# Optimization experiments

Measured on AMD Instinct MI355X. Metric: run time of the kernel, lower is better.

The kernel has to match this reference:

```python
import jax, jax.numpy as jnp
import numpy as np

N = 50000      # nodes
E = 800000     # edges
F_IN = 256
H1, D1 = 4, 32   # conv1 heads, per-head dim (hidden_features)
H2, D2 = 1, 32   # conv2 heads, per-head dim (out_features)
NEG_SLOPE = 0.2


def setup_inputs():
    key = jax.random.key(0)
    ks = jax.random.split(key, 12)
    x = jax.random.normal(ks[0], (N, F_IN), dtype=jnp.float32)
    src = jax.random.randint(ks[1], (E,), 0, N, dtype=jnp.int32)
    dst = jax.random.randint(ks[2], (E,), 0, N, dtype=jnp.int32)
    s = 0.05
    W1 = jax.random.normal(ks[3], (F_IN, H1 * D1), dtype=jnp.float32) * s
    al1 = jax.random.normal(ks[4], (H1, D1), dtype=jnp.float32) * s
    ar1 = jax.random.normal(ks[5], (H1, D1), dtype=jnp.float32) * s
    b1 = jnp.zeros((H1 * D1,), dtype=jnp.float32)
    W2 = jax.random.normal(ks[6], (H1 * D1, H2 * D2), dtype=jnp.float32) * s
    al2 = jax.random.normal(ks[7], (H2, D2), dtype=jnp.float32) * s
    ar2 = jax.random.normal(ks[8], (H2, D2), dtype=jnp.float32) * s
    b2 = jnp.zeros((H2 * D2,), dtype=jnp.float32)
    return {"x": x, "W1": W1, "al1": al1, "ar1": ar1, "b1": b1,
            "W2": W2, "al2": al2, "ar2": ar2, "b2": b2,
            "src": src, "dst": dst}


def gat_layer(x, W, al, ar, b, src, dst, H, D):
    # x: [N, F] -> feat: [N, H, D]
    feat = (x @ W).reshape(-1, H, D)
    el = jnp.sum(feat * al, axis=-1)   # [N, H]
    er = jnp.sum(feat * ar, axis=-1)   # [N, H]
    # per-edge attention logits, LeakyReLU
    e = jax.nn.leaky_relu(el[src] + er[dst], negative_slope=NEG_SLOPE)  # [E, H]
    # edge softmax over destination neighborhoods (stable)
    m = jax.ops.segment_max(e, dst, num_segments=N)          # [N, H]
    m = jnp.where(jnp.isfinite(m), m, 0.0)                   # guard zero-in-degree
    ee = jnp.exp(e - m[dst])                                 # [E, H]
    z = jax.ops.segment_sum(ee, dst, num_segments=N)         # [N, H]
    a = ee / jnp.maximum(z[dst], 1e-16)                      # [E, H]
    # weighted message aggregation
    msg = feat[src] * a[:, :, None]                          # [E, H, D]
    rst = jax.ops.segment_sum(msg, dst, num_segments=N)      # [N, H, D]
    return (rst + b.reshape(1, H, D)).reshape(-1, H * D)     # flatten(1)


def reference(x, W1, al1, ar1, b1, W2, al2, ar2, b2, src, dst):
    # dropouts are identity in eval mode; is_out_layer=True => no activation
    h = gat_layer(x, W1, al1, ar1, b1, src, dst, H1, D1)     # [N, H1*D1]
    out = gat_layer(h, W2, al2, ar2, b2, src, dst, H2, D2)   # [N, H2*D2]
    return out
```

## Files before the change

### kernel.cpp

```cpp
#include <hip/hip_runtime.h>

constexpr int F_IN = 256;
constexpr int H1 = 4, D1 = 32, F1 = H1 * D1;
constexpr int H2 = 1, D2 = 32, F2 = H2 * D2;
constexpr float NEG = 0.2f;

constexpr int BW = 128;
constexpr int NBUK_MAX = 512;
constexpr int CB = 128;

typedef short short8 __attribute__((ext_vector_type(8)));
typedef float f32x4 __attribute__((ext_vector_type(4)));

__device__ inline float bf2f(unsigned short u) {
    unsigned int x = ((unsigned int)u) << 16;
    return __builtin_bit_cast(float, x);
}
__device__ inline unsigned short f2bf(float f) {
    __bf16 h = (__bf16)f;
    return __builtin_bit_cast(unsigned short, h);
}

__global__ __launch_bounds__(256) void chist(const int* __restrict__ dst,
                                             unsigned int* __restrict__ Hc,
                                             int E, int nbuk) {
    __shared__ unsigned int h[NBUK_MAX];
    int tid = threadIdx.x;
    for (int i = tid; i < nbuk; i += 256) h[i] = 0;
    __syncthreads();
    int epb = (E + CB - 1) / CB;
    int e0 = blockIdx.x * epb, e1 = min(e0 + epb, E);
    for (int e = e0 + tid; e < e1; e += 256)
        atomicAdd(&h[dst[e] / BW], 1u);
    __syncthreads();
    for (int i = tid; i < nbuk; i += 256) Hc[(size_t)blockIdx.x * nbuk + i] = h[i];
}

__global__ __launch_bounds__(512) void bscan(const unsigned int* __restrict__ Hc,
                                             unsigned int* __restrict__ Bb,
                                             unsigned int* __restrict__ S, int nbuk) {
    __shared__ unsigned int tot[NBUK_MAX];
    int t = threadIdx.x;
    unsigned int run = 0;
    if (t < nbuk) {
        for (int b = 0; b < CB; ++b) {
            Bb[(size_t)b * nbuk + t] = run;
            run += Hc[(size_t)b * nbuk + t];
        }
    }
    tot[t] = (t < nbuk) ? run : 0;
    __syncthreads();
    for (int o = 1; o < NBUK_MAX; o <<= 1) {
        unsigned int v = (t >= o) ? tot[t - o] : 0;
        __syncthreads();
        tot[t] += v;
        __syncthreads();
    }
    if (t < nbuk) S[t] = tot[t] - run;
    if (t == nbuk - 1) S[nbuk] = tot[t];
}

__global__ __launch_bounds__(256) void cscat(const int* __restrict__ src,
                                             const int* __restrict__ dst,
                                             const unsigned int* __restrict__ Bb,
                                             const unsigned int* __restrict__ S,
                                             int2* __restrict__ pairs, int E, int nbuk) {
    __shared__ unsigned int h[NBUK_MAX];
    int tid = threadIdx.x;
    for (int i = tid; i < nbuk; i += 256) h[i] = 0;
    __syncthreads();
    int epb = (E + CB - 1) / CB;
    int e0 = blockIdx.x * epb, e1 = min(e0 + epb, E);
    const unsigned int* bb = Bb + (size_t)blockIdx.x * nbuk;
    for (int e = e0 + tid; e < e1; e += 256) {
        int d = dst[e];
        int k = d / BW;
        unsigned int r = atomicAdd(&h[k], 1u);
        unsigned int p = S[k] + bb[k] + r;
        pairs[p] = make_int2(src[e], d);
    }
}

__global__ __launch_bounds__(256) void fscat(const int2* __restrict__ pairs,
                                             const unsigned int* __restrict__ S,
                                             int* __restrict__ off, int* __restrict__ csr,
                                             int n, int E) {
    int k = blockIdx.x;
    int tid = threadIdx.x;
    unsigned int s0 = S[k], s1 = S[k + 1];
    __shared__ unsigned int cnt[BW];
    __shared__ unsigned int ex[BW];
    if (tid < BW) cnt[tid] = 0;
    __syncthreads();
    for (unsigned int i = s0 + tid; i < s1; i += 256)
        atomicAdd(&cnt[pairs[i].y - k * BW], 1u);
    __syncthreads();
    unsigned int orig = (tid < BW) ? cnt[tid] : 0;
    if (tid < BW) ex[tid] = orig;
    __syncthreads();
    for (int o = 1; o < BW; o <<= 1) {
        unsigned int v = (tid < BW && tid >= (unsigned)o) ? ex[tid - o] : 0;
        __syncthreads();
        if (tid < BW) ex[tid] += v;
        __syncthreads();
    }
    if (tid < BW) {
        ex[tid] -= orig;
        int node = k * BW + tid;
        if (node < n) off[node] = (int)(s0 + ex[tid]);
    }
    if (tid < BW) cnt[tid] = 0;
    __syncthreads();
    for (unsigned int i = s0 + tid; i < s1; i += 256) {
        int2 pr = pairs[i];
        int loc = pr.y - k * BW;
        unsigned int r = atomicAdd(&cnt[loc], 1u);
        csr[s0 + ex[loc] + r] = pr.x;
    }
    if (k == 0 && tid == 0) off[n] = E;
}

__global__ void wsplit_swz(const float* __restrict__ W,
                           unsigned short* __restrict__ Wh,
                           unsigned short* __restrict__ Wl, int K, int C) {
    int idx = blockIdx.x * 256 + threadIdx.x;
    if (idx >= K * C) return;
    int j    = idx & 7;
    int lane = (idx >> 3) & 63;
    int t    = idx >> 9;
    int FC   = C >> 4;
    int fc   = t % FC, ks = t / FC;
    int k = ks * 32 + (lane >> 4) * 8 + j;
    int c = fc * 16 + (lane & 15);
    float v = W[(size_t)k * C + c];
    __bf16 h = (__bf16)v;
    float hv = (float)h;
    __bf16 lo = (__bf16)(v - hv);
    Wh[idx] = __builtin_bit_cast(unsigned short, h);
    Wl[idx] = __builtin_bit_cast(unsigned short, lo);
}

constexpr int BM1 = 32;
__global__ __launch_bounds__(256) void gemm1_mfma(
    const float* __restrict__ X,
    const unsigned short* __restrict__ Wh,
    const unsigned short* __restrict__ Wl,
    unsigned short* __restrict__ outb, int n)
{
    __shared__ float xs[64 * BM1 * 4];
    const int tid  = threadIdx.x;
    const int lane = tid & 63;
    const int wid  = tid >> 6;
    const int wrow = (wid >> 1) * 16;
    const int wcol = (wid & 1) * 64;
    const int wc16 = wcol >> 4;
    const int row0 = blockIdx.x * BM1;
    const int l16  = lane & 15;
    const int khi  = lane >> 4;

    {
        int r = lane & 31;
        int sub = lane >> 5;
        int gr = row0 + r;
        gr = gr < n ? gr : (n - 1);
        const float* rowp = X + (size_t)gr * F_IN;
#pragma unroll
        for (int i = 0; i < 8; ++i) {
            int kc = wid * 16 + i * 2;
            const float* src = rowp + (kc + sub) * 4;
            float* dstf = &xs[kc * BM1 * 4];
            __builtin_amdgcn_global_load_lds(
                (const __attribute__((address_space(1))) unsigned int*)src,
                (__attribute__((address_space(3))) unsigned int*)dstf,
                16, 0, 0);
        }
    }
    asm volatile("s_waitcnt vmcnt(0)" ::: "memory");
    __syncthreads();

    f32x4 acc[4];
#pragma unroll
    for (int ni = 0; ni < 4; ++ni) acc[ni] = f32x4{0.f, 0.f, 0.f, 0.f};

    const int rt = wrow + l16;

#pragma unroll
    for (int ks = 0; ks < 8; ++ks) {
        const int kc = ks * 8 + khi * 2;

        short8 bh[4], bl[4];
#pragma unroll
        for (int ni = 0; ni < 4; ++ni) {
            int base = ((ks * 8 + wc16 + ni) * 64 + lane) * 8;
            bh[ni] = *(const short8*)(Wh + base);
            bl[ni] = *(const short8*)(Wl + base);
        }

        float4 xa0 = *(const float4*)&xs[(kc + 0) * BM1 * 4 + rt * 4];
        float4 xa1 = *(const float4*)&xs[(kc + 1) * BM1 * 4 + rt * 4];
        float v[8] = {xa0.x, xa0.y, xa0.z, xa0.w, xa1.x, xa1.y, xa1.z, xa1.w};
        short8 ah, al;
#pragma unroll
        for (int j = 0; j < 8; ++j) {
            __bf16 h = (__bf16)v[j];
            float hv = (float)h;
            __bf16 lo = (__bf16)(v[j] - hv);
            ah[j] = __builtin_bit_cast(short, h);
            al[j] = __builtin_bit_cast(short, lo);
        }

#pragma unroll
        for (int ni = 0; ni < 4; ++ni) {
            acc[ni] = __builtin_amdgcn_mfma_f32_16x16x32_bf16(al, bh[ni], acc[ni], 0, 0, 0);
            acc[ni] = __builtin_amdgcn_mfma_f32_16x16x32_bf16(ah, bl[ni], acc[ni], 0, 0, 0);
            acc[ni] = __builtin_amdgcn_mfma_f32_16x16x32_bf16(ah, bh[ni], acc[ni], 0, 0, 0);
        }
    }

    int rbase = row0 + wrow + khi * 4;
#pragma unroll
    for (int rr = 0; rr < 4; ++rr) {
        int row = rbase + rr;
        if (row < n) {
#pragma unroll
            for (int ni = 0; ni < 4; ++ni)
                outb[(size_t)row * F1 + wcol + ni * 16 + l16] = f2bf(acc[ni][rr]);
        }
    }
}

constexpr int BM2 = 64;
__global__ __launch_bounds__(256) void gemm2_mfma(
    const float* __restrict__ X,
    const unsigned short* __restrict__ Wh,
    const unsigned short* __restrict__ Wl,
    float* __restrict__ out, int n)
{
    __shared__ float xs[32 * BM2 * 4];
    const int tid  = threadIdx.x;
    const int lane = tid & 63;
    const int wid  = tid >> 6;
    const int wrow = wid * 16;
    const int row0 = blockIdx.x * BM2;
    const int l16  = lane & 15;
    const int khi  = lane >> 4;

    {
        int gr = row0 + lane;
        gr = gr < n ? gr : (n - 1);
        const float* rowp = X + (size_t)gr * F1;
#pragma unroll
        for (int i = 0; i < 8; ++i) {
            int kc = wid * 8 + i;
            const float* src = rowp + kc * 4;
            float* dstf = &xs[kc * BM2 * 4];
            __builtin_amdgcn_global_load_lds(
                (const __attribute__((address_space(1))) unsigned int*)src,
                (__attribute__((address_space(3))) unsigned int*)dstf,
                16, 0, 0);
        }
    }
    asm volatile("s_waitcnt vmcnt(0)" ::: "memory");
    __syncthreads();

    f32x4 acc[2];
#pragma unroll
    for (int ni = 0; ni < 2; ++ni) acc[ni] = f32x4{0.f, 0.f, 0.f, 0.f};

    const int rt = wrow + l16;

#pragma unroll
    for (int ks = 0; ks < 4; ++ks) {
        const int kc = ks * 8 + khi * 2;

        short8 bh[2], bl[2];
#pragma unroll
        for (int ni = 0; ni < 2; ++ni) {
            int base = ((ks * 2 + ni) * 64 + lane) * 8;
            bh[ni] = *(const short8*)(Wh + base);
            bl[ni] = *(const short8*)(Wl + base);
        }

        float4 xa0 = *(const float4*)&xs[(kc + 0) * BM2 * 4 + rt * 4];
        float4 xa1 = *(const float4*)&xs[(kc + 1) * BM2 * 4 + rt * 4];
        float v[8] = {xa0.x, xa0.y, xa0.z, xa0.w, xa1.x, xa1.y, xa1.z, xa1.w};
        short8 ah, al;
#pragma unroll
        for (int j = 0; j < 8; ++j) {
            __bf16 h = (__bf16)v[j];
            float hv = (float)h;
            __bf16 lo = (__bf16)(v[j] - hv);
            ah[j] = __builtin_bit_cast(short, h);
            al[j] = __builtin_bit_cast(short, lo);
        }

#pragma unroll
        for (int ni = 0; ni < 2; ++ni) {
            acc[ni] = __builtin_amdgcn_mfma_f32_16x16x32_bf16(al, bh[ni], acc[ni], 0, 0, 0);
            acc[ni] = __builtin_amdgcn_mfma_f32_16x16x32_bf16(ah, bl[ni], acc[ni], 0, 0, 0);
            acc[ni] = __builtin_amdgcn_mfma_f32_16x16x32_bf16(ah, bh[ni], acc[ni], 0, 0, 0);
        }
    }

    int rbase = row0 + wrow + khi * 4;
#pragma unroll
    for (int rr = 0; rr < 4; ++rr) {
        int row = rbase + rr;
        if (row < n) {
#pragma unroll
            for (int ni = 0; ni < 2; ++ni)
                out[(size_t)row * F2 + ni * 16 + l16] = acc[ni][rr];
        }
    }
}

template <int F, int H>
__global__ __launch_bounds__(256) void elr_bf16(const unsigned short* __restrict__ featb,
                                                const float* __restrict__ al,
                                                const float* __restrict__ ar,
                                                float* __restrict__ el,
                                                float* __restrict__ er, int n)
{
    constexpr int LPN = F / 4;
    constexpr int NPW = 64 / LPN;
    int wid = (blockIdx.x * 256 + threadIdx.x) >> 6;
    int lane = threadIdx.x & 63;
    int node = wid * NPW + lane / LPN;
    int l2 = lane % LPN;
    int c0 = l2 * 4;
    if (node >= n) return;
    ushort4 u = *(const ushort4*)(featb + (size_t)node * F + c0);
    float f0 = bf2f(u.x), f1 = bf2f(u.y), f2 = bf2f(u.z), f3 = bf2f(u.w);
    float4 a = *(const float4*)(al + c0);
    float4 r = *(const float4*)(ar + c0);
    float pel = f0 * a.x + f1 * a.y + f2 * a.z + f3 * a.w;
    float per = f0 * r.x + f1 * r.y + f2 * r.z + f3 * r.w;
#pragma unroll
    for (int o = 1; o < 8; o <<= 1) {
        pel += __shfl_xor(pel, o);
        per += __shfl_xor(per, o);
    }
    if ((l2 & 7) == 0) {
        int h = c0 / 32;
        el[(size_t)node * H + h] = pel;
        er[(size_t)node * H + h] = per;
    }
}

template <int F, int H>
__global__ __launch_bounds__(256) void elr_kernel(const float* __restrict__ feat,
                                                  const float* __restrict__ al,
                                                  const float* __restrict__ ar,
                                                  float* __restrict__ el,
                                                  float* __restrict__ er, int n)
{
    constexpr int LPN = F / 2;
    constexpr int NPW = 64 / LPN;
    int wid = (blockIdx.x * 256 + threadIdx.x) >> 6;
    int lane = threadIdx.x & 63;
    int node = wid * NPW + lane / LPN;
    int l2 = lane % LPN;
    int c0 = l2 * 2;
    if (node >= n) return;
    float2 f = *(const float2*)(feat + (size_t)node * F + c0);
    float2 a = *(const float2*)(al + c0);
    float2 r = *(const float2*)(ar + c0);
    float pel = f.x * a.x + f.y * a.y;
    float per = f.x * r.x + f.y * r.y;
#pragma unroll
    for (int o = 1; o < 16; o <<= 1) {
        pel += __shfl_xor(pel, o);
        per += __shfl_xor(per, o);
    }
    if ((l2 & 15) == 0) {
        int h = c0 / 32;
        el[(size_t)node * H + h] = pel;
        er[(size_t)node * H + h] = per;
    }
}

__global__ __launch_bounds__(256) void agg1_kernel(
    const int* __restrict__ off, const int* __restrict__ csr_src,
    const unsigned short* __restrict__ featb, const float* __restrict__ el,
    const float* __restrict__ er, const float* __restrict__ b,
    float* __restrict__ out, int n)
{
    int wid = (blockIdx.x * 256 + threadIdx.x) >> 6;
    int lane = threadIdx.x & 63;
    if (wid >= n) return;
    int c0 = (lane & 31) * 4;
    int h = (lane & 31) >> 3;
    int half = lane >> 5;
    float erv = er[(size_t)wid * H1 + h];
    float sw = 0.f;
    float4 acc = {0.f, 0.f, 0.f, 0.f};
    int jb = off[wid], je = off[wid + 1];
    int j = jb + half;
    for (; j + 6 < je; j += 8) {
        int s0 = csr_src[j];
        int s1 = csr_src[j + 2];
        int s2 = csr_src[j + 4];
        int s3 = csr_src[j + 6];
        ushort4 u0 = *(const ushort4*)(featb + (size_t)s0 * F1 + c0);
        ushort4 u1 = *(const ushort4*)(featb + (size_t)s1 * F1 + c0);
        ushort4 u2 = *(const ushort4*)(featb + (size_t)s2 * F1 + c0);
        ushort4 u3 = *(const ushort4*)(featb + (size_t)s3 * F1 + c0);
        float t0 = el[(size_t)s0 * H1 + h] + erv;
        float t1 = el[(size_t)s1 * H1 + h] + erv;
        float t2 = el[(size_t)s2 * H1 + h] + erv;
        float t3 = el[(size_t)s3 * H1 + h] + erv;
        t0 = t0 > 0.f ? t0 : NEG * t0;
        t1 = t1 > 0.f ? t1 : NEG * t1;
        t2 = t2 > 0.f ? t2 : NEG * t2;
        t3 = t3 > 0.f ? t3 : NEG * t3;
        float w0 = __expf(t0), w1 = __expf(t1), w2 = __expf(t2), w3 = __expf(t3);
        sw += (w0 + w1) + (w2 + w3);
        acc.x = fmaf(w0, bf2f(u0.x), fmaf(w1, bf2f(u1.x), fmaf(w2, bf2f(u2.x), fmaf(w3, bf2f(u3.x), acc.x))));
        acc.y = fmaf(w0, bf2f(u0.y), fmaf(w1, bf2f(u1.y), fmaf(w2, bf2f(u2.y), fmaf(w3, bf2f(u3.y), acc.y))));
        acc.z = fmaf(w0, bf2f(u0.z), fmaf(w1, bf2f(u1.z), fmaf(w2, bf2f(u2.z), fmaf(w3, bf2f(u3.z), acc.z))));
        acc.w = fmaf(w0, bf2f(u0.w), fmaf(w1, bf2f(u1.w), fmaf(w2, bf2f(u2.w), fmaf(w3, bf2f(u3.w), acc.w))));
    }
    for (; j < je; j += 2) {
        int s = csr_src[j];
        ushort4 u = *(const ushort4*)(featb + (size_t)s * F1 + c0);
        float t = el[(size_t)s * H1 + h] + erv;
        t = t > 0.f ? t : NEG * t;
        float w = __expf(t);
        sw += w;
        acc.x = fmaf(w, bf2f(u.x), acc.x);
        acc.y = fmaf(w, bf2f(u.y), acc.y);
        acc.z = fmaf(w, bf2f(u.z), acc.z);
        acc.w = fmaf(w, bf2f(u.w), acc.w);
    }
    acc.x += __shfl_xor(acc.x, 32);
    acc.y += __shfl_xor(acc.y, 32);
    acc.z += __shfl_xor(acc.z, 32);
    acc.w += __shfl_xor(acc.w, 32);
    sw    += __shfl_xor(sw, 32);
    if (half == 0) {
        float inv = 1.f / fmaxf(sw, 1e-16f);
        float4 bb = *(const float4*)(b + c0);
        float4 t = {acc.x * inv + bb.x, acc.y * inv + bb.y,
                    acc.z * inv + bb.z, acc.w * inv + bb.w};
        *(float4*)(out + (size_t)wid * F1 + c0) = t;
    }
}

__global__ __launch_bounds__(256) void agg2_kernel(
    const int* __restrict__ off, const int* __restrict__ csr_src,
    const float* __restrict__ feat, const float* __restrict__ el,
    const float* __restrict__ er, const float* __restrict__ b,
    float* __restrict__ out, int n)
{
    int wid = (blockIdx.x * 256 + threadIdx.x) >> 6;
    int lane = threadIdx.x & 63;
    if (wid >= n) return;
    int c0 = (lane & 7) * 4;
    int grp = lane >> 3;
    float erv = er[wid];
    float sw = 0.f;
    float4 acc = {0.f, 0.f, 0.f, 0.f};
    int jb = off[wid], je = off[wid + 1];
    int j = jb + grp;
    for (; j + 8 < je; j += 16) {
        int s0 = csr_src[j];
        int s1 = csr_src[j + 8];
        float4 f0 = *(const float4*)(feat + (size_t)s0 * F2 + c0);
        float4 f1 = *(const float4*)(feat + (size_t)s1 * F2 + c0);
        float t0 = el[s0] + erv;
        float t1 = el[s1] + erv;
        t0 = t0 > 0.f ? t0 : NEG * t0;
        t1 = t1 > 0.f ? t1 : NEG * t1;
        float w0 = __expf(t0);
        float w1 = __expf(t1);
        sw += w0 + w1;
        acc.x = fmaf(w0, f0.x, fmaf(w1, f1.x, acc.x));
        acc.y = fmaf(w0, f0.y, fmaf(w1, f1.y, acc.y));
        acc.z = fmaf(w0, f0.z, fmaf(w1, f1.z, acc.z));
        acc.w = fmaf(w0, f0.w, fmaf(w1, f1.w, acc.w));
    }
    for (; j < je; j += 8) {
        int s = csr_src[j];
        float4 f = *(const float4*)(feat + (size_t)s * F2 + c0);
        float t = el[s] + erv;
        t = t > 0.f ? t : NEG * t;
        float w = __expf(t);
        sw += w;
        acc.x = fmaf(w, f.x, acc.x);
        acc.y = fmaf(w, f.y, acc.y);
        acc.z = fmaf(w, f.z, acc.z);
        acc.w = fmaf(w, f.w, acc.w);
    }
#pragma unroll
    for (int o = 8; o < 64; o <<= 1) {
        acc.x += __shfl_xor(acc.x, o);
        acc.y += __shfl_xor(acc.y, o);
        acc.z += __shfl_xor(acc.z, o);
        acc.w += __shfl_xor(acc.w, o);
        sw    += __shfl_xor(sw, o);
    }
    if (lane < 8) {
        float inv = 1.f / fmaxf(sw, 1e-16f);
        float4 bb = *(const float4*)(b + c0);
        float4 t = {acc.x * inv + bb.x, acc.y * inv + bb.y,
                    acc.z * inv + bb.z, acc.w * inv + bb.w};
        *(float4*)(out + (size_t)wid * F2 + c0) = t;
    }
}

extern "C" void kernel_launch(void* const* d_in, const int* in_sizes, int n_in,
                              void* d_out, int out_size, void* d_ws, size_t ws_size,
                              hipStream_t stream) {
    const float* x   = (const float*)d_in[0];
    const float* W1  = (const float*)d_in[1];
    const float* al1 = (const float*)d_in[2];
    const float* ar1 = (const float*)d_in[3];
    const float* b1  = (const float*)d_in[4];
    const float* W2  = (const float*)d_in[5];
    const float* al2 = (const float*)d_in[6];
    const float* ar2 = (const float*)d_in[7];
    const float* b2  = (const float*)d_in[8];
    const int*   src = (const int*)d_in[9];
    const int*   dst = (const int*)d_in[10];

    const int N = in_sizes[0] / F_IN;
    const int E = in_sizes[9];
    const int NBUK = (N + BW - 1) / BW;

    char* w = (char*)d_ws;
    size_t o = 0;
    auto alloc = [&](size_t bytes) { size_t cur = o; o += (bytes + 255) & ~255ULL; return cur; };
    int*   off   = (int*)  (w + alloc((size_t)(N + 1) * 4));
    int*   csr   = (int*)  (w + alloc((size_t)E * 4));
    int2*  pairs = (int2*) (w + alloc((size_t)E * 8));
    unsigned int* Hc = (unsigned int*)(w + alloc((size_t)CB * NBUK * 4));
    unsigned int* Bb = (unsigned int*)(w + alloc((size_t)CB * NBUK * 4));
    unsigned int* S  = (unsigned int*)(w + alloc((size_t)(NBUK + 1) * 4));
    unsigned short* feat1b = (unsigned short*)(w + alloc((size_t)N * F1 * 2));
    float* el1   = (float*)(w + alloc((size_t)N * H1 * 4));
    float* er1   = (float*)(w + alloc((size_t)N * H1 * 4));
    float* h1    = (float*)(w + alloc((size_t)N * F1 * 4));
    float* feat2 = (float*)(w + alloc((size_t)N * F2 * 4));
    float* el2   = (float*)(w + alloc((size_t)N * H2 * 4));
    float* er2   = (float*)(w + alloc((size_t)N * H2 * 4));
    unsigned short* W1h = (unsigned short*)(w + alloc((size_t)F_IN * F1 * 2));
    unsigned short* W1l = (unsigned short*)(w + alloc((size_t)F_IN * F1 * 2));
    unsigned short* W2h = (unsigned short*)(w + alloc((size_t)F1 * F2 * 2));
    unsigned short* W2l = (unsigned short*)(w + alloc((size_t)F1 * F2 * 2));
    (void)ws_size; (void)n_in; (void)out_size;

    chist<<<CB, 256, 0, stream>>>(dst, Hc, E, NBUK);
    bscan<<<1, 512, 0, stream>>>(Hc, Bb, S, NBUK);
    cscat<<<CB, 256, 0, stream>>>(src, dst, Bb, S, pairs, E, NBUK);
    fscat<<<NBUK, 256, 0, stream>>>(pairs, S, off, csr, N, E);

    wsplit_swz<<<(F_IN * F1 + 255) / 256, 256, 0, stream>>>(W1, W1h, W1l, F_IN, F1);
    wsplit_swz<<<(F1 * F2 + 255) / 256, 256, 0, stream>>>(W2, W2h, W2l, F1, F2);

    gemm1_mfma<<<(N + BM1 - 1) / BM1, 256, 0, stream>>>(x, W1h, W1l, feat1b, N);
    elr_bf16<F1, H1><<<(N + 7) / 8, 256, 0, stream>>>(feat1b, al1, ar1, el1, er1, N);
    agg1_kernel<<<(N + 3) / 4, 256, 0, stream>>>(off, csr, feat1b, el1, er1, b1, h1, N);

    gemm2_mfma<<<(N + BM2 - 1) / BM2, 256, 0, stream>>>(h1, W2h, W2l, feat2, N);
    elr_kernel<F2, H2><<<(N + 15) / 16, 256, 0, stream>>>(feat2, al2, ar2, el2, er2, N);
    agg2_kernel<<<(N + 3) / 4, 256, 0, stream>>>(off, csr, feat2, el2, er2, b2, (float*)d_out, N);
}
```

Before: 155.1 us.

## Fuse attention logits into GEMM epilogues and compact CSR build intermediates

The el/er attention-logit dot products move into the epilogues of both MFMA GEMMs, reduced across lanes with shuffles. This removes two separate kernels that re-read the feature matrices. The CSR build packs (local dst, src) into one 32-bit word instead of an int2, which halves the pairs traffic; this relies on src < 2^17 and BW=128. The histogram is stored transposed so the bucket scan reads it with vector loads, and the two weight-split kernels are merged into one launch. The costs are extra epilogue work and register pressure in the GEMMs, plus an implicit limit on node count from the packing.

Measured after the change: 149.7 us. 1.04x faster.

```diff
diff --git a/kernel.cpp b/kernel.cpp
--- a/kernel.cpp
+++ b/kernel.cpp
@@ -22,7 +22,7 @@
 }
 
 __global__ __launch_bounds__(256) void chist(const int* __restrict__ dst,
-                                             unsigned int* __restrict__ Hc,
+                                             unsigned int* __restrict__ HcT,
                                              int E, int nbuk) {
     __shared__ unsigned int h[NBUK_MAX];
     int tid = threadIdx.x;
@@ -31,21 +31,27 @@
     int epb = (E + CB - 1) / CB;
     int e0 = blockIdx.x * epb, e1 = min(e0 + epb, E);
     for (int e = e0 + tid; e < e1; e += 256)
-        atomicAdd(&h[dst[e] / BW], 1u);
-    __syncthreads();
-    for (int i = tid; i < nbuk; i += 256) Hc[(size_t)blockIdx.x * nbuk + i] = h[i];
-}
-
-__global__ __launch_bounds__(512) void bscan(const unsigned int* __restrict__ Hc,
+        atomicAdd(&h[dst[e] >> 7], 1u);
+    __syncthreads();
+    for (int i = tid; i < nbuk; i += 256) HcT[(size_t)i * CB + blockIdx.x] = h[i];
+}
+
+__global__ __launch_bounds__(512) void bscan(const unsigned int* __restrict__ HcT,
                                              unsigned int* __restrict__ Bb,
                                              unsigned int* __restrict__ S, int nbuk) {
     __shared__ unsigned int tot[NBUK_MAX];
     int t = threadIdx.x;
     unsigned int run = 0;
     if (t < nbuk) {
-        for (int b = 0; b < CB; ++b) {
-            Bb[(size_t)b * nbuk + t] = run;
-            run += Hc[(size_t)b * nbuk + t];
+        const uint4* row = (const uint4*)(HcT + (size_t)t * CB);
+#pragma unroll 8
+        for (int b4 = 0; b4 < CB / 4; ++b4) {
+            uint4 v = row[b4];
+            int b = b4 * 4;
+            Bb[(size_t)(b + 0) * nbuk + t] = run; run += v.x;
+            Bb[(size_t)(b + 1) * nbuk + t] = run; run += v.y;
+            Bb[(size_t)(b + 2) * nbuk + t] = run; run += v.z;
+            Bb[(size_t)(b + 3) * nbuk + t] = run; run += v.w;
         }
     }
     tot[t] = (t < nbuk) ? run : 0;
@@ -64,7 +70,7 @@
                                              const int* __restrict__ dst,
                                              const unsigned int* __restrict__ Bb,
                                              const unsigned int* __restrict__ S,
-                                             int2* __restrict__ pairs, int E, int nbuk) {
+                                             unsigned int* __restrict__ pairs, int E, int nbuk) {
     __shared__ unsigned int h[NBUK_MAX];
     int tid = threadIdx.x;
     for (int i = tid; i < nbuk; i += 256) h[i] = 0;
@@ -74,14 +80,14 @@
     const unsigned int* bb = Bb + (size_t)blockIdx.x * nbuk;
     for (int e = e0 + tid; e < e1; e += 256) {
         int d = dst[e];
-        int k = d / BW;
+        int k = d >> 7;
         unsigned int r = atomicAdd(&h[k], 1u);
         unsigned int p = S[k] + bb[k] + r;
-        pairs[p] = make_int2(src[e], d);
-    }
-}
-
-__global__ __launch_bounds__(256) void fscat(const int2* __restrict__ pairs,
+        pairs[p] = ((unsigned int)(d & 127) << 17) | (unsigned int)src[e];
+    }
+}
+
+__global__ __launch_bounds__(256) void fscat(const unsigned int* __restrict__ pairs,
                                              const unsigned int* __restrict__ S,
                                              int* __restrict__ off, int* __restrict__ csr,
                                              int n, int E) {
@@ -93,7 +99,7 @@
     if (tid < BW) cnt[tid] = 0;
     __syncthreads();
     for (unsigned int i = s0 + tid; i < s1; i += 256)
-        atomicAdd(&cnt[pairs[i].y - k * BW], 1u);
+        atomicAdd(&cnt[pairs[i] >> 17], 1u);
     __syncthreads();
     unsigned int orig = (tid < BW) ? cnt[tid] : 0;
     if (tid < BW) ex[tid] = orig;
@@ -112,19 +118,16 @@
     if (tid < BW) cnt[tid] = 0;
     __syncthreads();
     for (unsigned int i = s0 + tid; i < s1; i += 256) {
-        int2 pr = pairs[i];
-        int loc = pr.y - k * BW;
+        unsigned int pr = pairs[i];
+        int loc = pr >> 17;
         unsigned int r = atomicAdd(&cnt[loc], 1u);
-        csr[s0 + ex[loc] + r] = pr.x;
+        csr[s0 + ex[loc] + r] = (int)(pr & 0x1FFFFu);
     }
     if (k == 0 && tid == 0) off[n] = E;
 }
 
-__global__ void wsplit_swz(const float* __restrict__ W,
-                           unsigned short* __restrict__ Wh,
-                           unsigned short* __restrict__ Wl, int K, int C) {
-    int idx = blockIdx.x * 256 + threadIdx.x;
-    if (idx >= K * C) return;
+__device__ inline void wsplit_one(const float* W, unsigned short* Wh, unsigned short* Wl,
+                                  int idx, int C) {
     int j    = idx & 7;
     int lane = (idx >> 3) & 63;
     int t    = idx >> 9;
@@ -139,13 +142,24 @@
     Wh[idx] = __builtin_bit_cast(unsigned short, h);
     Wl[idx] = __builtin_bit_cast(unsigned short, lo);
 }
+__global__ void wsplit_swz2(const float* __restrict__ W1, unsigned short* __restrict__ W1h,
+                            unsigned short* __restrict__ W1l,
+                            const float* __restrict__ W2, unsigned short* __restrict__ W2h,
+                            unsigned short* __restrict__ W2l) {
+    int idx = blockIdx.x * 256 + threadIdx.x;
+    constexpr int N1 = F_IN * F1;
+    if (idx < N1) wsplit_one(W1, W1h, W1l, idx, F1);
+    else if (idx < N1 + F1 * F2) wsplit_one(W2, W2h, W2l, idx - N1, F2);
+}
 
 constexpr int BM1 = 32;
 __global__ __launch_bounds__(256) void gemm1_mfma(
     const float* __restrict__ X,
     const unsigned short* __restrict__ Wh,
     const unsigned short* __restrict__ Wl,
-    unsigned short* __restrict__ outb, int n)
+    const float* __restrict__ alv, const float* __restrict__ arv,
+    unsigned short* __restrict__ outb,
+    float* __restrict__ el, float* __restrict__ er, int n)
 {
     __shared__ float xs[64 * BM1 * 4];
     const int tid  = threadIdx.x;
@@ -167,10 +181,10 @@
 #pragma unroll
         for (int i = 0; i < 8; ++i) {
             int kc = wid * 16 + i * 2;
-            const float* src = rowp + (kc + sub) * 4;
+            const float* srcp = rowp + (kc + sub) * 4;
             float* dstf = &xs[kc * BM1 * 4];
             __builtin_amdgcn_global_load_lds(
-                (const __attribute__((address_space(1))) unsigned int*)src,
+                (const __attribute__((address_space(1))) unsigned int*)srcp,
                 (__attribute__((address_space(3))) unsigned int*)dstf,
                 16, 0, 0);
         }
@@ -199,32 +213,58 @@
         float4 xa0 = *(const float4*)&xs[(kc + 0) * BM1 * 4 + rt * 4];
         float4 xa1 = *(const float4*)&xs[(kc + 1) * BM1 * 4 + rt * 4];
         float v[8] = {xa0.x, xa0.y, xa0.z, xa0.w, xa1.x, xa1.y, xa1.z, xa1.w};
-        short8 ah, al;
+        short8 ah, al8;
 #pragma unroll
         for (int j = 0; j < 8; ++j) {
             __bf16 h = (__bf16)v[j];
             float hv = (float)h;
             __bf16 lo = (__bf16)(v[j] - hv);
             ah[j] = __builtin_bit_cast(short, h);
-            al[j] = __builtin_bit_cast(short, lo);
+            al8[j] = __builtin_bit_cast(short, lo);
         }
 
 #pragma unroll
         for (int ni = 0; ni < 4; ++ni) {
-            acc[ni] = __builtin_amdgcn_mfma_f32_16x16x32_bf16(al, bh[ni], acc[ni], 0, 0, 0);
+            acc[ni] = __builtin_amdgcn_mfma_f32_16x16x32_bf16(al8, bh[ni], acc[ni], 0, 0, 0);
             acc[ni] = __builtin_amdgcn_mfma_f32_16x16x32_bf16(ah, bl[ni], acc[ni], 0, 0, 0);
             acc[ni] = __builtin_amdgcn_mfma_f32_16x16x32_bf16(ah, bh[ni], acc[ni], 0, 0, 0);
         }
     }
 
+    const int hh0 = wcol >> 5;
+    float alr[2][2], arr[2][2];
+#pragma unroll
+    for (int t = 0; t < 2; ++t) {
+        int head = hh0 + t;
+        alr[t][0] = alv[head * 32 + l16];
+        alr[t][1] = alv[head * 32 + 16 + l16];
+        arr[t][0] = arv[head * 32 + l16];
+        arr[t][1] = arv[head * 32 + 16 + l16];
+    }
+
     int rbase = row0 + wrow + khi * 4;
 #pragma unroll
     for (int rr = 0; rr < 4; ++rr) {
         int row = rbase + rr;
-        if (row < n) {
+        bool ok = row < n;
+        if (ok) {
 #pragma unroll
             for (int ni = 0; ni < 4; ++ni)
                 outb[(size_t)row * F1 + wcol + ni * 16 + l16] = f2bf(acc[ni][rr]);
+        }
+#pragma unroll
+        for (int t = 0; t < 2; ++t) {
+            float pel = acc[2 * t][rr] * alr[t][0] + acc[2 * t + 1][rr] * alr[t][1];
+            float per = acc[2 * t][rr] * arr[t][0] + acc[2 * t + 1][rr] * arr[t][1];
+#pragma unroll
+            for (int o = 1; o < 16; o <<= 1) {
+                pel += __shfl_xor(pel, o);
+                per += __shfl_xor(per, o);
+            }
+            if (ok && l16 == 0) {
+                el[(size_t)row * H1 + hh0 + t] = pel;
+                er[(size_t)row * H1 + hh0 + t] = per;
+            }
         }
     }
 }
@@ -234,7 +274,9 @@
     const float* __restrict__ X,
     const unsigned short* __restrict__ Wh,
     const unsigned short* __restrict__ Wl,
-    float* __restrict__ out, int n)
+    const float* __restrict__ alv, const float* __restrict__ arv,
+    float* __restrict__ out,
+    float* __restrict__ el, float* __restrict__ er, int n)
 {
     __shared__ float xs[32 * BM2 * 4];
     const int tid  = threadIdx.x;
@@ -252,10 +294,10 @@
 #pragma unroll
         for (int i = 0; i < 8; ++i) {
             int kc = wid * 8 + i;
-            const float* src = rowp + kc * 4;
+            const float* srcp = rowp + kc * 4;
             float* dstf = &xs[kc * BM2 * 4];
             __builtin_amdgcn_global_load_lds(
-                (const __attribute__((address_space(1))) unsigned int*)src,
+                (const __attribute__((address_space(1))) unsigned int*)srcp,
                 (__attribute__((address_space(3))) unsigned int*)dstf,
                 16, 0, 0);
         }
@@ -284,98 +326,48 @@
         float4 xa0 = *(const float4*)&xs[(kc + 0) * BM2 * 4 + rt * 4];
         float4 xa1 = *(const float4*)&xs[(kc + 1) * BM2 * 4 + rt * 4];
         float v[8] = {xa0.x, xa0.y, xa0.z, xa0.w, xa1.x, xa1.y, xa1.z, xa1.w};
-        short8 ah, al;
+        short8 ah, al8;
 #pragma unroll
         for (int j = 0; j < 8; ++j) {
             __bf16 h = (__bf16)v[j];
             float hv = (float)h;
             __bf16 lo = (__bf16)(v[j] - hv);
             ah[j] = __builtin_bit_cast(short, h);
-            al[j] = __builtin_bit_cast(short, lo);
+            al8[j] = __builtin_bit_cast(short, lo);
         }
 
 #pragma unroll
         for (int ni = 0; ni < 2; ++ni) {
-            acc[ni] = __builtin_amdgcn_mfma_f32_16x16x32_bf16(al, bh[ni], acc[ni], 0, 0, 0);
+            acc[ni] = __builtin_amdgcn_mfma_f32_16x16x32_bf16(al8, bh[ni], acc[ni], 0, 0, 0);
             acc[ni] = __builtin_amdgcn_mfma_f32_16x16x32_bf16(ah, bl[ni], acc[ni], 0, 0, 0);
             acc[ni] = __builtin_amdgcn_mfma_f32_16x16x32_bf16(ah, bh[ni], acc[ni], 0, 0, 0);
         }
     }
 
+    float al0 = alv[l16], al1c = alv[16 + l16];
+    float ar0 = arv[l16], ar1c = arv[16 + l16];
+
     int rbase = row0 + wrow + khi * 4;
 #pragma unroll
     for (int rr = 0; rr < 4; ++rr) {
         int row = rbase + rr;
-        if (row < n) {
+        bool ok = row < n;
+        if (ok) {
 #pragma unroll
             for (int ni = 0; ni < 2; ++ni)
                 out[(size_t)row * F2 + ni * 16 + l16] = acc[ni][rr];
         }
-    }
-}
-
-template <int F, int H>
-__global__ __launch_bounds__(256) void elr_bf16(const unsigned short* __restrict__ featb,
-                                                const float* __restrict__ al,
-                                                const float* __restrict__ ar,
-                                                float* __restrict__ el,
-                                                float* __restrict__ er, int n)
-{
-    constexpr int LPN = F / 4;
-    constexpr int NPW = 64 / LPN;
-    int wid = (blockIdx.x * 256 + threadIdx.x) >> 6;
-    int lane = threadIdx.x & 63;
-    int node = wid * NPW + lane / LPN;
-    int l2 = lane % LPN;
-    int c0 = l2 * 4;
-    if (node >= n) return;
-    ushort4 u = *(const ushort4*)(featb + (size_t)node * F + c0);
-    float f0 = bf2f(u.x), f1 = bf2f(u.y), f2 = bf2f(u.z), f3 = bf2f(u.w);
-    float4 a = *(const float4*)(al + c0);
-    float4 r = *(const float4*)(ar + c0);
-    float pel = f0 * a.x + f1 * a.y + f2 * a.z + f3 * a.w;
-    float per = f0 * r.x + f1 * r.y + f2 * r.z + f3 * r.w;
-#pragma unroll
-    for (int o = 1; o < 8; o <<= 1) {
-        pel += __shfl_xor(pel, o);
-        per += __shfl_xor(per, o);
-    }
-    if ((l2 & 7) == 0) {
-        int h = c0 / 32;
-        el[(size_t)node * H + h] = pel;
-        er[(size_t)node * H + h] = per;
-    }
-}
-
-template <int F, int H>
-__global__ __launch_bounds__(256) void elr_kernel(const float* __restrict__ feat,
-                                                  const float* __restrict__ al,
-                                                  const float* __restrict__ ar,
-                                                  float* __restrict__ el,
-                                                  float* __restrict__ er, int n)
-{
-    constexpr int LPN = F / 2;
-    constexpr int NPW = 64 / LPN;
-    int wid = (blockIdx.x * 256 + threadIdx.x) >> 6;
-    int lane = threadIdx.x & 63;
-    int node = wid * NPW + lane / LPN;
-    int l2 = lane % LPN;
-    int c0 = l2 * 2;
-    if (node >= n) return;
-    float2 f = *(const float2*)(feat + (size_t)node * F + c0);
-    float2 a = *(const float2*)(al + c0);
-    float2 r = *(const float2*)(ar + c0);
-    float pel = f.x * a.x + f.y * a.y;
-    float per = f.x * r.x + f.y * r.y;
-#pragma unroll
-    for (int o = 1; o < 16; o <<= 1) {
-        pel += __shfl_xor(pel, o);
-        per += __shfl_xor(per, o);
-    }
-    if ((l2 & 15) == 0) {
-        int h = c0 / 32;
-        el[(size_t)node * H + h] = pel;
-        er[(size_t)node * H + h] = per;
+        float pel = acc[0][rr] * al0 + acc[1][rr] * al1c;
+        float per = acc[0][rr] * ar0 + acc[1][rr] * ar1c;
+#pragma unroll
+        for (int o = 1; o < 16; o <<= 1) {
+            pel += __shfl_xor(pel, o);
+            per += __shfl_xor(per, o);
+        }
+        if (ok && l16 == 0) {
+            el[row] = pel;
+            er[row] = per;
+        }
     }
 }
 
@@ -532,10 +524,10 @@
     auto alloc = [&](size_t bytes) { size_t cur = o; o += (bytes + 255) & ~255ULL; return cur; };
     int*   off   = (int*)  (w + alloc((size_t)(N + 1) * 4));
     int*   csr   = (int*)  (w + alloc((size_t)E * 4));
-    int2*  pairs = (int2*) (w + alloc((size_t)E * 8));
-    unsigned int* Hc = (unsigned int*)(w + alloc((size_t)CB * NBUK * 4));
-    unsigned int* Bb = (unsigned int*)(w + alloc((size_t)CB * NBUK * 4));
-    unsigned int* S  = (unsigned int*)(w + alloc((size_t)(NBUK + 1) * 4));
+    unsigned int* pairs = (unsigned int*)(w + alloc((size_t)E * 4));
+    unsigned int* HcT = (unsigned int*)(w + alloc((size_t)CB * NBUK * 4));
+    unsigned int* Bb  = (unsigned int*)(w + alloc((size_t)CB * NBUK * 4));
+    unsigned int* S   = (unsigned int*)(w + alloc((size_t)(NBUK + 1) * 4));
     unsigned short* feat1b = (unsigned short*)(w + alloc((size_t)N * F1 * 2));
     float* el1   = (float*)(w + alloc((size_t)N * H1 * 4));
     float* er1   = (float*)(w + alloc((size_t)N * H1 * 4));
@@ -549,19 +541,19 @@
     unsigned short* W2l = (unsigned short*)(w + alloc((size_t)F1 * F2 * 2));
     (void)ws_size; (void)n_in; (void)out_size;
 
-    chist<<<CB, 256, 0, stream>>>(dst, Hc, E, NBUK);
-    bscan<<<1, 512, 0, stream>>>(Hc, Bb, S, NBUK);
+    chist<<<CB, 256, 0, stream>>>(dst, HcT, E, NBUK);
+    bscan<<<1, 512, 0, stream>>>(HcT, Bb, S, NBUK);
     cscat<<<CB, 256, 0, stream>>>(src, dst, Bb, S, pairs, E, NBUK);
     fscat<<<NBUK, 256, 0, stream>>>(pairs, S, off, csr, N, E);
 
-    wsplit_swz<<<(F_IN * F1 + 255) / 256, 256, 0, stream>>>(W1, W1h, W1l, F_IN, F1);
-    wsplit_swz<<<(F1 * F2 + 255) / 256, 256, 0, stream>>>(W2, W2h, W2l, F1, F2);
-
-    gemm1_mfma<<<(N + BM1 - 1) / BM1, 256, 0, stream>>>(x, W1h, W1l, feat1b, N);
-    elr_bf16<F1, H1><<<(N + 7) / 8, 256, 0, stream>>>(feat1b, al1, ar1, el1, er1, N);
+    wsplit_swz2<<<(F_IN * F1 + F1 * F2 + 255) / 256, 256, 0, stream>>>(
+        W1, W1h, W1l, W2, W2h, W2l);
+
+    gemm1_mfma<<<(N + BM1 - 1) / BM1, 256, 0, stream>>>(
+        x, W1h, W1l, al1, ar1, feat1b, el1, er1, N);
     agg1_kernel<<<(N + 3) / 4, 256, 0, stream>>>(off, csr, feat1b, el1, er1, b1, h1, N);
 
-    gemm2_mfma<<<(N + BM2 - 1) / BM2, 256, 0, stream>>>(h1, W2h, W2l, feat2, N);
-    elr_kernel<F2, H2><<<(N + 15) / 16, 256, 0, stream>>>(feat2, al2, ar2, el2, er2, N);
+    gemm2_mfma<<<(N + BM2 - 1) / BM2, 256, 0, stream>>>(
+        h1, W2h, W2l, al2, ar2, feat2, el2, er2, N);
     agg2_kernel<<<(N + 3) / 4, 256, 0, stream>>>(off, csr, feat2, el2, er2, b2, (float*)d_out, N);
 }
```
